# Optimization experiments

Hardware: AMD Instinct MI355X
Metric: run time of the kernel (lower is better)

Reference implementation:

```python
import jax, jax.numpy as jnp
import numpy as np

B, T, D, DS = 8, 4096, 1024, 64


def setup_inputs() -> dict:
    key = jax.random.key(0)
    ks = jax.random.split(key, 9)
    s = 0.02
    return {
        "x": jax.random.normal(ks[0], (B, T, D), dtype=jnp.float32),
        "Wq": jax.random.normal(ks[1], (DS, D), dtype=jnp.float32) * s,
        "bq": jnp.zeros((DS,), dtype=jnp.float32),
        "Wk": jax.random.normal(ks[2], (DS, D), dtype=jnp.float32) * s,
        "bk": jnp.zeros((DS,), dtype=jnp.float32),
        "Wv": jax.random.normal(ks[3], (DS, D), dtype=jnp.float32) * s,
        "bv": jnp.zeros((DS,), dtype=jnp.float32),
        "decay": jnp.full((DS,), 0.95, dtype=jnp.float32),
        "Wo": jax.random.normal(ks[4], (D, DS), dtype=jnp.float32) * s,
        "bo": jnp.zeros((D,), dtype=jnp.float32),
    }


def reference(x, Wq, bq, Wk, bk, Wv, bv, decay, Wo, bo):
    # projections: [B,T,DS]
    q = jnp.einsum('btd,sd->bts', x, Wq) + bq
    k = jnp.einsum('btd,sd->bts', x, Wk) + bk
    v = jnp.einsum('btd,sd->bts', x, Wv) + bv
    d = jax.nn.sigmoid(decay)  # [DS]

    def step(S, qkv_t):
        q_t, k_t, v_t = qkv_t  # each [B, DS]
        # diag(d) @ S + v k^T  (rank-1 update per batch)
        S = d[None, :, None] * S + v_t[:, :, None] * k_t[:, None, :]
        o = jnp.einsum('bij,bj->bi', S, q_t)
        return S, o

    S0 = jnp.zeros((x.shape[0], d.shape[0], d.shape[0]), dtype=x.dtype)
    qkv = (jnp.swapaxes(q, 0, 1), jnp.swapaxes(k, 0, 1), jnp.swapaxes(v, 0, 1))  # [T,B,DS]
    _, outs = jax.lax.scan(step, S0, qkv)  # outs: [T,B,DS]
    scan_out = jnp.swapaxes(outs, 0, 1)  # [B,T,DS]
    return x + jnp.einsum('bts,ds->btd', scan_out, Wo) + bo
```

## Files before the change

### kernel.cpp

```cpp
#include <hip/hip_runtime.h>
#include <cstdint>
#include <cstddef>
#include <cmath>

#define Bb 8
#define Tt 4096
#define Dd 1024
#define DS 64
#define Mm (Bb*Tt)
#define PAD 68

typedef __bf16 bf16x8 __attribute__((ext_vector_type(8)));
typedef __bf16 bf16x4v __attribute__((ext_vector_type(4)));
typedef float f32x4 __attribute__((ext_vector_type(4)));

__device__ __forceinline__ float4* ldsP(float* buf, int row, int col4) {
  return (float4*)(buf + row * PAD + (((col4) ^ ((row >> 3) & 7)) << 2));
}

__global__ __launch_bounds__(256) void convert_w(
    const float* __restrict__ Wq, const float* __restrict__ Wk,
    const float* __restrict__ Wv, const float* __restrict__ Wo,
    __bf16* __restrict__ Wqkvb, __bf16* __restrict__ Wob)
{
  int idx = blockIdx.x * 256 + threadIdx.x;
  if (idx < 196608) {
    float v = (idx < 65536) ? Wq[idx]
            : (idx < 131072) ? Wk[idx - 65536] : Wv[idx - 131072];
    Wqkvb[idx] = (__bf16)v;
  }
  if (idx < 65536) Wob[idx] = (__bf16)Wo[idx];
}

__global__ __launch_bounds__(256) void qkv_mfma(
    const float* __restrict__ x, const __bf16* __restrict__ Wb,
    const float* __restrict__ bq, const float* __restrict__ bk,
    const float* __restrict__ bv, float* __restrict__ qkv)
{
  const int w  = threadIdx.x >> 6;
  const int l  = threadIdx.x & 63;
  const int m0 = blockIdx.x * 64;
  const int c0 = w * 48;
  const int lr = l & 15;
  const int lk = l >> 4;

  f32x4 acc[4][3] = {};

  const float*  ax = x  + (size_t)(m0 + lr) * 1024 + lk * 8;
  const __bf16* bw = Wb + (size_t)(c0 + lr) * 1024 + lk * 8;

  for (int k0 = 0; k0 < 1024; k0 += 32) {
    bf16x8 a[4], b[3];
    #pragma unroll
    for (int mf = 0; mf < 4; ++mf) {
      const float* p = ax + (size_t)mf * 16 * 1024 + k0;
      float4 f0 = *(const float4*)p;
      float4 f1 = *(const float4*)(p + 4);
      bf16x8 t;
      t[0] = (__bf16)f0.x; t[1] = (__bf16)f0.y;
      t[2] = (__bf16)f0.z; t[3] = (__bf16)f0.w;
      t[4] = (__bf16)f1.x; t[5] = (__bf16)f1.y;
      t[6] = (__bf16)f1.z; t[7] = (__bf16)f1.w;
      a[mf] = t;
    }
    #pragma unroll
    for (int nf = 0; nf < 3; ++nf)
      b[nf] = *(const bf16x8*)(bw + (size_t)nf * 16 * 1024 + k0);
    #pragma unroll
    for (int mf = 0; mf < 4; ++mf)
      #pragma unroll
      for (int nf = 0; nf < 3; ++nf)
        acc[mf][nf] = __builtin_amdgcn_mfma_f32_16x16x32_bf16(
            a[mf], b[nf], acc[mf][nf], 0, 0, 0);
  }

  float bias[3];
  #pragma unroll
  for (int nf = 0; nf < 3; ++nf) {
    int j = c0 + nf * 16 + lr;
    bias[nf] = (j < 64) ? bq[j] : (j < 128) ? bk[j - 64] : bv[j - 128];
  }

  #pragma unroll
  for (int mf = 0; mf < 4; ++mf)
    #pragma unroll
    for (int nf = 0; nf < 3; ++nf) {
      int j = c0 + nf * 16 + lr;
      #pragma unroll
      for (int r = 0; r < 4; ++r) {
        int m = m0 + mf * 16 + lk * 4 + r;
        qkv[(size_t)m * 192 + j] = acc[mf][nf][r] + bias[nf];
      }
    }
}

__global__ __launch_bounds__(256) void scan_chunk_a(
    const float* __restrict__ qkv, const float* __restrict__ decay,
    float* __restrict__ Ubuf, float* __restrict__ so)
{
  __shared__ float Qs[64 * PAD];
  __shared__ float Ks[64 * PAD];
  __shared__ float Vs[64 * PAD];
  __shared__ float l2d[64];

  const int tid = threadIdx.x;
  const int bc  = blockIdx.x;
  const int b   = bc >> 6;
  const int ch  = bc & 63;
  const int ti  = tid >> 4;
  const int tj  = tid & 15;

  const float* base = qkv + ((size_t)(b * Tt + ch * 64)) * 192;

  #pragma unroll
  for (int it = 0; it < 12; ++it) {
    int idx = tid + it * 256;
    int row = idx / 48, f = idx % 48;
    float4 g = *(const float4*)(base + (size_t)row * 192 + f * 4);
    float4* dst;
    if (f < 16)      dst = ldsP(Qs, row, f);
    else if (f < 32) dst = ldsP(Ks, row, f - 16);
    else             dst = ldsP(Vs, row, f - 32);
    *dst = g;
  }
  if (tid < 64) {
    float d = 1.0f / (1.0f + expf(-decay[tid]));
    l2d[tid] = log2f(d);
  }
  __syncthreads();

  {
    int s = tid >> 2;
    #pragma unroll
    for (int g4 = 0; g4 < 4; ++g4) {
      int col4 = (tid & 3) * 4 + g4;
      float4* p = ldsP(Vs, s, col4);
      float4 v = *p;
      float e0 = exp2f(-(float)s * l2d[col4 * 4 + 0]);
      float e1 = exp2f(-(float)s * l2d[col4 * 4 + 1]);
      float e2 = exp2f(-(float)s * l2d[col4 * 4 + 2]);
      float e3 = exp2f(-(float)s * l2d[col4 * 4 + 3]);
      v.x *= e0; v.y *= e1; v.z *= e2; v.w *= e3;
      *p = v;
    }
  }

  float gval[4][4] = {};
  #pragma unroll
  for (int kk4 = 0; kk4 < 16; ++kk4) {
    float4 K4[4], Q4[4];
    #pragma unroll
    for (int r = 0; r < 4; ++r) K4[r] = *ldsP(Ks, ti * 4 + r, kk4);
    #pragma unroll
    for (int c = 0; c < 4; ++c) Q4[c] = *ldsP(Qs, tj * 4 + c, kk4);
    #pragma unroll
    for (int r = 0; r < 4; ++r)
      #pragma unroll
      for (int c = 0; c < 4; ++c) {
        gval[r][c] = fmaf(K4[r].x, Q4[c].x, gval[r][c]);
        gval[r][c] = fmaf(K4[r].y, Q4[c].y, gval[r][c]);
        gval[r][c] = fmaf(K4[r].z, Q4[c].z, gval[r][c]);
        gval[r][c] = fmaf(K4[r].w, Q4[c].w, gval[r][c]);
      }
  }
  #pragma unroll
  for (int r = 0; r < 4; ++r)
    #pragma unroll
    for (int c = 0; c < 4; ++c)
      if (ti * 4 + r > tj * 4 + c) gval[r][c] = 0.0f;

  __syncthreads();

  #pragma unroll
  for (int r = 0; r < 4; ++r) {
    float4 g4 = {gval[r][0], gval[r][1], gval[r][2], gval[r][3]};
    *ldsP(Qs, ti * 4 + r, tj) = g4;
  }
  __syncthreads();

  float uacc[4][4] = {};
  float oacc[4][4] = {};
  for (int s = 0; s < 64; ++s) {
    float4 Vti = *ldsP(Vs, s, ti);
    float4 Ktj = *ldsP(Ks, s, tj);
    float4 Gti = *ldsP(Qs, s, ti);
    float4 Vtj = *ldsP(Vs, s, tj);
    const float vi[4] = {Vti.x, Vti.y, Vti.z, Vti.w};
    const float kj[4] = {Ktj.x, Ktj.y, Ktj.z, Ktj.w};
    const float gu[4] = {Gti.x, Gti.y, Gti.z, Gti.w};
    const float vj[4] = {Vtj.x, Vtj.y, Vtj.z, Vtj.w};
    #pragma unroll
    for (int r = 0; r < 4; ++r)
      #pragma unroll
      for (int c = 0; c < 4; ++c) {
        uacc[r][c] = fmaf(vi[r], kj[c], uacc[r][c]);
        oacc[r][c] = fmaf(gu[r], vj[c], oacc[r][c]);
      }
  }

  #pragma unroll
  for (int r = 0; r < 4; ++r) {
    int i = ti * 4 + r;
    float d63 = exp2f(63.0f * l2d[i]);
    float4 o = {uacc[r][0] * d63, uacc[r][1] * d63,
                uacc[r][2] * d63, uacc[r][3] * d63};
    *(float4*)(Ubuf + ((size_t)bc * 64 + i) * 64 + tj * 4) = o;
  }
  #pragma unroll
  for (int r = 0; r < 4; ++r) {
    int u = ti * 4 + r;
    float e0 = exp2f((float)u * l2d[tj * 4 + 0]);
    float e1 = exp2f((float)u * l2d[tj * 4 + 1]);
    float e2 = exp2f((float)u * l2d[tj * 4 + 2]);
    float e3 = exp2f((float)u * l2d[tj * 4 + 3]);
    float4 o = {oacc[r][0] * e0, oacc[r][1] * e1,
                oacc[r][2] * e2, oacc[r][3] * e3};
    *(float4*)(so + ((size_t)(b * Tt + ch * 64 + u)) * 64 + tj * 4) = o;
  }
}

__global__ __launch_bounds__(256) void scan_state(
    const float* __restrict__ decay, float* __restrict__ Ubuf)
{
  const int b  = blockIdx.x >> 2;
  const int jq = blockIdx.x & 3;
  const int i  = threadIdx.x >> 2;
  const int j4 = threadIdx.x & 3;

  float d = 1.0f / (1.0f + expf(-decay[i]));
  float d2 = d * d, d4 = d2 * d2, d8 = d4 * d4;
  float d16 = d8 * d8, d32 = d16 * d16, d64 = d32 * d32;

  float* base = Ubuf + ((size_t)b * 64) * 4096 + (size_t)i * 64 + jq * 16 + j4 * 4;

  float4 S = {0.f, 0.f, 0.f, 0.f};
  float4 u0 = *(const float4*)(base + 0 * 4096);
  float4 u1 = *(const float4*)(base + 1 * 4096);
  float4 u2 = *(const float4*)(base + 2 * 4096);
  float4 u3 = *(const float4*)(base + 3 * 4096);

  for (int c = 0; c < 64; c += 4) {
    float4 n0 = u0, n1 = u1, n2 = u2, n3 = u3;
    if (c + 4 < 64) {
      n0 = *(const float4*)(base + (size_t)(c + 4) * 4096);
      n1 = *(const float4*)(base + (size_t)(c + 5) * 4096);
      n2 = *(const float4*)(base + (size_t)(c + 6) * 4096);
      n3 = *(const float4*)(base + (size_t)(c + 7) * 4096);
    }
    *(float4*)(base + (size_t)(c + 0) * 4096) = S;
    S.x = fmaf(d64, S.x, u0.x); S.y = fmaf(d64, S.y, u0.y);
    S.z = fmaf(d64, S.z, u0.z); S.w = fmaf(d64, S.w, u0.w);
    *(float4*)(base + (size_t)(c + 1) * 4096) = S;
    S.x = fmaf(d64, S.x, u1.x); S.y = fmaf(d64, S.y, u1.y);
    S.z = fmaf(d64, S.z, u1.z); S.w = fmaf(d64, S.w, u1.w);
    *(float4*)(base + (size_t)(c + 2) * 4096) = S;
    S.x = fmaf(d64, S.x, u2.x); S.y = fmaf(d64, S.y, u2.y);
    S.z = fmaf(d64, S.z, u2.z); S.w = fmaf(d64, S.w, u2.w);
    *(float4*)(base + (size_t)(c + 3) * 4096) = S;
    S.x = fmaf(d64, S.x, u3.x); S.y = fmaf(d64, S.y, u3.y);
    S.z = fmaf(d64, S.z, u3.z); S.w = fmaf(d64, S.w, u3.w);
    u0 = n0; u1 = n1; u2 = n2; u3 = n3;
  }
}

__global__ __launch_bounds__(256) void scan_chunk_c(
    const float* __restrict__ qkv, const float* __restrict__ decay,
    const float* __restrict__ Sbuf, const float* __restrict__ so,
    __bf16* __restrict__ sob)
{
  __shared__ float Ss[64 * PAD];
  __shared__ float Qs[64 * PAD];
  __shared__ float l2d[64];

  const int tid = threadIdx.x;
  const int bc  = blockIdx.x;
  const int b   = bc >> 6;
  const int ch  = bc & 63;
  const int ti  = tid >> 4;
  const int tj  = tid & 15;

  #pragma unroll
  for (int it = 0; it < 4; ++it) {
    int idx = tid + it * 256;
    int row = idx >> 4, col4 = idx & 15;
    float4 s4 = *(const float4*)(Sbuf + (size_t)bc * 4096 + (size_t)row * 64 + col4 * 4);
    *ldsP(Ss, row, col4) = s4;
    float4 q4 = *(const float4*)(qkv + ((size_t)(b * Tt + ch * 64 + row)) * 192 + col4 * 4);
    *ldsP(Qs, row, col4) = q4;
  }
  if (tid < 64) {
    float d = 1.0f / (1.0f + expf(-decay[tid]));
    l2d[tid] = log2f(d);
  }
  __syncthreads();

  float acc[4][4] = {};
  #pragma unroll
  for (int j4 = 0; j4 < 16; ++j4) {
    float4 Q4[4], S4[4];
    #pragma unroll
    for (int r = 0; r < 4; ++r) Q4[r] = *ldsP(Qs, ti * 4 + r, j4);
    #pragma unroll
    for (int c = 0; c < 4; ++c) S4[c] = *ldsP(Ss, tj * 4 + c, j4);
    #pragma unroll
    for (int r = 0; r < 4; ++r)
      #pragma unroll
      for (int c = 0; c < 4; ++c) {
        acc[r][c] = fmaf(Q4[r].x, S4[c].x, acc[r][c]);
        acc[r][c] = fmaf(Q4[r].y, S4[c].y, acc[r][c]);
        acc[r][c] = fmaf(Q4[r].z, S4[c].z, acc[r][c]);
        acc[r][c] = fmaf(Q4[r].w, S4[c].w, acc[r][c]);
      }
  }

  #pragma unroll
  for (int r = 0; r < 4; ++r) {
    int u = ti * 4 + r;
    size_t row = (size_t)(b * Tt + ch * 64 + u);
    float4 prev = *(const float4*)(so + row * 64 + tj * 4);
    float e0 = exp2f((float)(u + 1) * l2d[tj * 4 + 0]);
    float e1 = exp2f((float)(u + 1) * l2d[tj * 4 + 1]);
    float e2 = exp2f((float)(u + 1) * l2d[tj * 4 + 2]);
    float e3 = exp2f((float)(u + 1) * l2d[tj * 4 + 3]);
    bf16x4v ov;
    ov[0] = (__bf16)fmaf(acc[r][0], e0, prev.x);
    ov[1] = (__bf16)fmaf(acc[r][1], e1, prev.y);
    ov[2] = (__bf16)fmaf(acc[r][2], e2, prev.z);
    ov[3] = (__bf16)fmaf(acc[r][3], e3, prev.w);
    *(bf16x4v*)(sob + row * 64 + tj * 4) = ov;
  }
}

__global__ __launch_bounds__(256) void out_mfma(
    const float* __restrict__ x, const __bf16* __restrict__ sob,
    const __bf16* __restrict__ Wob, const float* __restrict__ bo,
    float* __restrict__ out)
{
  const int bid = blockIdx.x;
  const int rb  = bid >> 3;
  const int cb  = bid & 7;
  const int w   = threadIdx.x >> 6;
  const int l   = threadIdx.x & 63;
  const int wr  = w >> 1;
  const int wc  = w & 1;
  const int m0  = rb * 128 + wr * 64;
  const int c0  = cb * 128 + wc * 64;
  const int lr  = l & 15;
  const int lk  = l >> 4;

  f32x4 acc[4][4] = {};

  const __bf16* ap = sob + (size_t)(m0 + lr) * 64 + lk * 8;
  const __bf16* bp = Wob + (size_t)(c0 + lr) * 64 + lk * 8;

  #pragma unroll
  for (int ks = 0; ks < 2; ++ks) {
    bf16x8 a[4], b[4];
    #pragma unroll
    for (int mf = 0; mf < 4; ++mf)
      a[mf] = *(const bf16x8*)(ap + (size_t)mf * 16 * 64 + ks * 32);
    #pragma unroll
    for (int nf = 0; nf < 4; ++nf)
      b[nf] = *(const bf16x8*)(bp + (size_t)nf * 16 * 64 + ks * 32);
    #pragma unroll
    for (int mf = 0; mf < 4; ++mf)
      #pragma unroll
      for (int nf = 0; nf < 4; ++nf)
        acc[mf][nf] = __builtin_amdgcn_mfma_f32_16x16x32_bf16(
            a[mf], b[nf], acc[mf][nf], 0, 0, 0);
  }

  #pragma unroll
  for (int nf = 0; nf < 4; ++nf) {
    int j = c0 + nf * 16 + lr;
    float bj = bo[j];
    #pragma unroll
    for (int mf = 0; mf < 4; ++mf) {
      #pragma unroll
      for (int r = 0; r < 4; ++r) {
        size_t m = (size_t)m0 + mf * 16 + lk * 4 + r;
        out[m * 1024 + j] = x[m * 1024 + j] + acc[mf][nf][r] + bj;
      }
    }
  }
}

extern "C" void kernel_launch(void* const* d_in, const int* in_sizes, int n_in,
                              void* d_out, int out_size, void* d_ws, size_t ws_size,
                              hipStream_t stream)
{
  const float* x   = (const float*)d_in[0];
  const float* Wq  = (const float*)d_in[1];
  const float* bq  = (const float*)d_in[2];
  const float* Wk  = (const float*)d_in[3];
  const float* bk  = (const float*)d_in[4];
  const float* Wv  = (const float*)d_in[5];
  const float* bv  = (const float*)d_in[6];
  const float* dec = (const float*)d_in[7];
  const float* Wo  = (const float*)d_in[8];
  const float* bo  = (const float*)d_in[9];
  float* out = (float*)d_out;

  float*  qkv   = (float*)d_ws;
  float*  so    = qkv + (size_t)Mm * 192;
  float*  Ubuf  = so + (size_t)Mm * 64;
  __bf16* sob   = (__bf16*)(Ubuf + (size_t)512 * 4096);
  __bf16* Wqkvb = sob + (size_t)Mm * 64;
  __bf16* Wob   = Wqkvb + (size_t)192 * 1024;

  convert_w<<<768, 256, 0, stream>>>(Wq, Wk, Wv, Wo, Wqkvb, Wob);
  qkv_mfma<<<Mm / 64, 256, 0, stream>>>(x, Wqkvb, bq, bk, bv, qkv);
  scan_chunk_a<<<512, 256, 0, stream>>>(qkv, dec, Ubuf, so);
  scan_state<<<32, 256, 0, stream>>>(dec, Ubuf);
  scan_chunk_c<<<512, 256, 0, stream>>>(qkv, dec, Ubuf, so, sob);
  out_mfma<<<2048, 256, 0, stream>>>(x, sob, Wob, bo, out);
}
```

Baseline: 431.1 us.

## Transpose MFMA operands for vectorized stores and stage x tile through LDS

Both GEMM kernels swap the MFMA A/B operands so each lane's accumulator holds four consecutive output columns. This lets the epilogues use float4 stores and float4 loads of x and bias instead of scalar strided accesses. The QKV projection also converts x to bf16 once per block into a swizzled LDS tile, prefetching the next k-chunk into registers. Previously each of the four waves reloaded and reconverted the same x rows from global memory. The cost is two barriers per k-step and extra LDS traffic.

Result: faster. 388.7 us (-9.8%).

```diff
diff --git a/kernel.cpp b/kernel.cpp
--- a/kernel.cpp
+++ b/kernel.cpp
@@ -37,61 +37,87 @@
     const float* __restrict__ bq, const float* __restrict__ bk,
     const float* __restrict__ bv, float* __restrict__ qkv)
 {
-  const int w  = threadIdx.x >> 6;
-  const int l  = threadIdx.x & 63;
-  const int m0 = blockIdx.x * 64;
-  const int c0 = w * 48;
-  const int lr = l & 15;
-  const int lk = l >> 4;
-
-  f32x4 acc[4][3] = {};
-
-  const float*  ax = x  + (size_t)(m0 + lr) * 1024 + lk * 8;
-  const __bf16* bw = Wb + (size_t)(c0 + lr) * 1024 + lk * 8;
-
-  for (int k0 = 0; k0 < 1024; k0 += 32) {
-    bf16x8 a[4], b[3];
+  __shared__ __bf16 xs[64 * 64];
+
+  const int tid = threadIdx.x;
+  const int w   = tid >> 6;
+  const int l   = tid & 63;
+  const int m0  = blockIdx.x * 64;
+  const int c0  = w * 48;
+  const int lr  = l & 15;
+  const int lk  = l >> 4;
+
+  const int srow = tid & 63;
+  const int sk   = (tid >> 6) * 16;
+  const float* xsrc = x + (size_t)(m0 + srow) * 1024 + sk;
+  const int wb0 = srow * 128 + ((sk * 2 + 0)  ^ ((srow & 7) << 4));
+  const int wb1 = srow * 128 + ((sk * 2 + 16) ^ ((srow & 7) << 4));
+
+  f32x4 acc[3][4] = {};
+
+  float4 f0 = *(const float4*)(xsrc + 0);
+  float4 f1 = *(const float4*)(xsrc + 4);
+  float4 f2 = *(const float4*)(xsrc + 8);
+  float4 f3 = *(const float4*)(xsrc + 12);
+
+  for (int k0 = 0; k0 < 1024; k0 += 64) {
+    bf16x8 h0, h1;
+    h0[0] = (__bf16)f0.x; h0[1] = (__bf16)f0.y; h0[2] = (__bf16)f0.z; h0[3] = (__bf16)f0.w;
+    h0[4] = (__bf16)f1.x; h0[5] = (__bf16)f1.y; h0[6] = (__bf16)f1.z; h0[7] = (__bf16)f1.w;
+    h1[0] = (__bf16)f2.x; h1[1] = (__bf16)f2.y; h1[2] = (__bf16)f2.z; h1[3] = (__bf16)f2.w;
+    h1[4] = (__bf16)f3.x; h1[5] = (__bf16)f3.y; h1[6] = (__bf16)f3.z; h1[7] = (__bf16)f3.w;
+
+    __syncthreads();
+    *(bf16x8*)((char*)xs + wb0) = h0;
+    *(bf16x8*)((char*)xs + wb1) = h1;
+    __syncthreads();
+
+    if (k0 + 64 < 1024) {
+      f0 = *(const float4*)(xsrc + k0 + 64);
+      f1 = *(const float4*)(xsrc + k0 + 68);
+      f2 = *(const float4*)(xsrc + k0 + 72);
+      f3 = *(const float4*)(xsrc + k0 + 76);
+    }
+
+    #pragma unroll
+    for (int ks = 0; ks < 2; ++ks) {
+      bf16x8 wf[3], xf[4];
+      #pragma unroll
+      for (int jf = 0; jf < 3; ++jf)
+        wf[jf] = *(const bf16x8*)(Wb + (size_t)(c0 + jf * 16 + lr) * 1024
+                                     + k0 + ks * 32 + lk * 8);
+      #pragma unroll
+      for (int mf = 0; mf < 4; ++mf) {
+        int row = mf * 16 + lr;
+        int boff = row * 128 + ((ks * 64 + lk * 16) ^ ((row & 7) << 4));
+        xf[mf] = *(const bf16x8*)((const char*)xs + boff);
+      }
+      #pragma unroll
+      for (int jf = 0; jf < 3; ++jf)
+        #pragma unroll
+        for (int mf = 0; mf < 4; ++mf)
+          acc[jf][mf] = __builtin_amdgcn_mfma_f32_16x16x32_bf16(
+              wf[jf], xf[mf], acc[jf][mf], 0, 0, 0);
+    }
+  }
+
+  #pragma unroll
+  for (int jf = 0; jf < 3; ++jf) {
+    int j0 = c0 + jf * 16 + lk * 4;
+    const float* bsrc = (j0 < 64) ? (bq + j0)
+                      : (j0 < 128) ? (bk + j0 - 64) : (bv + j0 - 128);
+    float4 b4 = *(const float4*)bsrc;
     #pragma unroll
     for (int mf = 0; mf < 4; ++mf) {
-      const float* p = ax + (size_t)mf * 16 * 1024 + k0;
-      float4 f0 = *(const float4*)p;
-      float4 f1 = *(const float4*)(p + 4);
-      bf16x8 t;
-      t[0] = (__bf16)f0.x; t[1] = (__bf16)f0.y;
-      t[2] = (__bf16)f0.z; t[3] = (__bf16)f0.w;
-      t[4] = (__bf16)f1.x; t[5] = (__bf16)f1.y;
-      t[6] = (__bf16)f1.z; t[7] = (__bf16)f1.w;
-      a[mf] = t;
-    }
-    #pragma unroll
-    for (int nf = 0; nf < 3; ++nf)
-      b[nf] = *(const bf16x8*)(bw + (size_t)nf * 16 * 1024 + k0);
-    #pragma unroll
-    for (int mf = 0; mf < 4; ++mf)
-      #pragma unroll
-      for (int nf = 0; nf < 3; ++nf)
-        acc[mf][nf] = __builtin_amdgcn_mfma_f32_16x16x32_bf16(
-            a[mf], b[nf], acc[mf][nf], 0, 0, 0);
-  }
-
-  float bias[3];
-  #pragma unroll
-  for (int nf = 0; nf < 3; ++nf) {
-    int j = c0 + nf * 16 + lr;
-    bias[nf] = (j < 64) ? bq[j] : (j < 128) ? bk[j - 64] : bv[j - 128];
-  }
-
-  #pragma unroll
-  for (int mf = 0; mf < 4; ++mf)
-    #pragma unroll
-    for (int nf = 0; nf < 3; ++nf) {
-      int j = c0 + nf * 16 + lr;
-      #pragma unroll
-      for (int r = 0; r < 4; ++r) {
-        int m = m0 + mf * 16 + lk * 4 + r;
-        qkv[(size_t)m * 192 + j] = acc[mf][nf][r] + bias[nf];
-      }
-    }
+      int m = m0 + mf * 16 + lr;
+      float4 o;
+      o.x = acc[jf][mf][0] + b4.x;
+      o.y = acc[jf][mf][1] + b4.y;
+      o.z = acc[jf][mf][2] + b4.z;
+      o.w = acc[jf][mf][3] + b4.w;
+      *(float4*)(qkv + (size_t)m * 192 + j0) = o;
+    }
+  }
 }
 
 __global__ __launch_bounds__(256) void scan_chunk_a(
@@ -350,37 +376,40 @@
 
   f32x4 acc[4][4] = {};
 
-  const __bf16* ap = sob + (size_t)(m0 + lr) * 64 + lk * 8;
-  const __bf16* bp = Wob + (size_t)(c0 + lr) * 64 + lk * 8;
+  const __bf16* ap = Wob + (size_t)(c0 + lr) * 64 + lk * 8;
+  const __bf16* bp = sob + (size_t)(m0 + lr) * 64 + lk * 8;
 
   #pragma unroll
   for (int ks = 0; ks < 2; ++ks) {
     bf16x8 a[4], b[4];
     #pragma unroll
+    for (int jf = 0; jf < 4; ++jf)
+      a[jf] = *(const bf16x8*)(ap + (size_t)jf * 16 * 64 + ks * 32);
+    #pragma unroll
     for (int mf = 0; mf < 4; ++mf)
-      a[mf] = *(const bf16x8*)(ap + (size_t)mf * 16 * 64 + ks * 32);
-    #pragma unroll
-    for (int nf = 0; nf < 4; ++nf)
-      b[nf] = *(const bf16x8*)(bp + (size_t)nf * 16 * 64 + ks * 32);
-    #pragma unroll
-    for (int mf = 0; mf < 4; ++mf)
-      #pragma unroll
-      for (int nf = 0; nf < 4; ++nf)
-        acc[mf][nf] = __builtin_amdgcn_mfma_f32_16x16x32_bf16(
-            a[mf], b[nf], acc[mf][nf], 0, 0, 0);
-  }
-
-  #pragma unroll
-  for (int nf = 0; nf < 4; ++nf) {
-    int j = c0 + nf * 16 + lr;
-    float bj = bo[j];
+      b[mf] = *(const bf16x8*)(bp + (size_t)mf * 16 * 64 + ks * 32);
+    #pragma unroll
+    for (int jf = 0; jf < 4; ++jf)
+      #pragma unroll
+      for (int mf = 0; mf < 4; ++mf)
+        acc[jf][mf] = __builtin_amdgcn_mfma_f32_16x16x32_bf16(
+            a[jf], b[mf], acc[jf][mf], 0, 0, 0);
+  }
+
+  #pragma unroll
+  for (int jf = 0; jf < 4; ++jf) {
+    int j0 = c0 + jf * 16 + lk * 4;
+    float4 b4 = *(const float4*)(bo + j0);
     #pragma unroll
     for (int mf = 0; mf < 4; ++mf) {
-      #pragma unroll
-      for (int r = 0; r < 4; ++r) {
-        size_t m = (size_t)m0 + mf * 16 + lk * 4 + r;
-        out[m * 1024 + j] = x[m * 1024 + j] + acc[mf][nf][r] + bj;
-      }
+      size_t m = (size_t)m0 + mf * 16 + lr;
+      float4 xv = *(const float4*)(x + m * 1024 + j0);
+      float4 o;
+      o.x = xv.x + acc[jf][mf][0] + b4.x;
+      o.y = xv.y + acc[jf][mf][1] + b4.y;
+      o.z = xv.z + acc[jf][mf][2] + b4.z;
+      o.w = xv.w + acc[jf][mf][3] + b4.w;
+      *(float4*)(out + m * 1024 + j0) = o;
     }
   }
 }
```
